# Kernel optimization log

Hardware: AMD Instinct MI355X
Metric: run time of the kernel (lower is better)

The kernel has to match this reference:

```python
import jax, jax.numpy as jnp
import numpy as np
import math

N_HEADS = 4


def setup_inputs() -> dict:
    key = jax.random.key(0)
    ks = jax.random.split(key, 5)
    Bs, M, T, C = 4, 190, 512, 64
    x = jax.random.normal(ks[0], (Bs, M, T, C), dtype=jnp.float32)
    s = 1.0 / math.sqrt(C)
    Wq = jax.random.normal(ks[1], (C, C), dtype=jnp.float32) * s
    Wk = jax.random.normal(ks[2], (C, C), dtype=jnp.float32) * s
    Wv = jax.random.normal(ks[3], (C, C), dtype=jnp.float32) * s
    Wp = jax.random.normal(ks[4], (C, C), dtype=jnp.float32) * s
    z = jnp.zeros((C,), dtype=jnp.float32)
    return {"x": x, "Wq": Wq, "bq": z, "Wk": Wk, "bk": z, "Wv": Wv, "bv": z, "Wp": Wp, "bp": z}


def reference(x, Wq, bq, Wk, bk, Wv, bv, Wp, bp):
    # AxialMultiAttention forward, tied=True, linear=False, dropout=0 (eval).
    Bs, M, T, C = x.shape
    N, D = N_HEADS, C // N_HEADS

    def heads(y):  # [Bs,M,T,C] -> [Bs,M,N,T,D]
        return y.reshape(Bs, M, T, N, D).transpose(0, 1, 3, 2, 4)

    q = heads(x @ Wq + bq)
    k = heads(x @ Wk + bk)
    v = heads(x @ Wv + bv)

    # tied: sum queries/keys over the axial (pair) dim M, keepdim -> size-1 axis
    q_t = q.sum(axis=1)  # [Bs,N,T,D]
    k_t = k.sum(axis=1)  # [Bs,N,T,D]
    scale = 1.0 / math.sqrt(D * M)
    weights = jax.nn.softmax(jnp.einsum('bnqd,bnkd->bnqk', q_t, k_t) * scale, axis=-1)  # [Bs,N,T,T]

    # broadcast tied weights across M when multiplying values
    att = jnp.einsum('bnqk,bmnkd->bmnqd', weights, v)  # [Bs,M,N,T,D]
    att = att.transpose(0, 1, 3, 2, 4).reshape(Bs, M, T, N * D)
    out = att @ Wp + bp  # [Bs,M,T,C]

    # a = weights.detach()[0].mean(0): weights has keepdim axis of size 1 in torch,
    # so [0] -> [1,N,T,T] and mean over dim 0 -> [N,T,T]
    a = jax.lax.stop_gradient(weights)[0]  # [N,T,T]
    return out, a
```

## Files before the change

kernel.cpp:

```cpp
#include <hip/hip_runtime.h>

typedef unsigned short ushort_t;
typedef __bf16 bf16x8 __attribute__((ext_vector_type(8)));
typedef float f32x4 __attribute__((ext_vector_type(4)));
typedef float f32x16 __attribute__((ext_vector_type(16)));

#define DEVI __device__ __forceinline__

constexpr int BSZ = 4;
constexpr int MDIM = 190;
constexpr int TDIM = 512;
constexpr int CDIM = 64;

DEVI ushort_t f2bf(float f) {
    union { float f; unsigned int u; } v; v.f = f;
    unsigned int u = v.u;
    u += 0x7FFFu + ((u >> 16) & 1u);
    return (ushort_t)(u >> 16);
}

__global__ __launch_bounds__(256, 4) void k_vproj(const float* __restrict__ x,
                                                  const float* __restrict__ Wv,
                                                  const float* __restrict__ bv,
                                                  ushort_t* __restrict__ vf,
                                                  float* __restrict__ xsp) {
    __shared__ __align__(16) ushort_t xbf[64 * 72];
    __shared__ __align__(16) ushort_t WvT[64 * 72];
    __shared__ __align__(16) ushort_t vst[64 * 72];

    int tid = threadIdx.x;
    int bid = blockIdx.x;
    int mg = bid & 15;
    int tt = (bid >> 4) & 7;
    int b = bid >> 7;
    int t0 = tt * 64;
    int mbase = mg * 12;
    int cnt = (mbase + 12 <= MDIM) ? 12 : (MDIM - mbase);

    int w = tid >> 6, lane = tid & 63;
    int la = lane & 15, lb = lane >> 4;
    int r = tid >> 2, seg = tid & 3;

    int chunk = tid >> 3, u = tid & 7;
    int ksr = chunk >> 3;
    int nn2 = (chunk >> 1) & 3;
    int lhi2 = chunk & 1;
    int d0 = u * 2;

#pragma unroll
    for (int rep = 0; rep < 16; ++rep) {
        int j = rep * 256 + tid;
        int ci = j >> 6, co = j & 63;
        WvT[co * 72 + ci] = f2bf(Wv[j]);
    }
    float bvv[4];
#pragma unroll
    for (int cf = 0; cf < 4; ++cf) bvv[cf] = bv[16 * cf + la];

    float xacc[16];
#pragma unroll
    for (int u2 = 0; u2 < 16; ++u2) xacc[u2] = 0.f;

    const size_t mstride = (size_t)TDIM * CDIM;
    size_t xaddr = ((size_t)(b * MDIM + mbase) * TDIM + t0 + r) * CDIM + seg * 16;

    float4 xv[4];
#pragma unroll
    for (int u2 = 0; u2 < 4; ++u2) xv[u2] = *(const float4*)(x + xaddr + u2 * 4);

    f32x4 zz = {0.f, 0.f, 0.f, 0.f};

    for (int i = 0; i < cnt; ++i) {
#pragma unroll
        for (int u2 = 0; u2 < 4; ++u2) {
            xacc[u2 * 4 + 0] += xv[u2].x;
            xacc[u2 * 4 + 1] += xv[u2].y;
            xacc[u2 * 4 + 2] += xv[u2].z;
            xacc[u2 * 4 + 3] += xv[u2].w;
            ushort4 h;
            h.x = f2bf(xv[u2].x); h.y = f2bf(xv[u2].y);
            h.z = f2bf(xv[u2].z); h.w = f2bf(xv[u2].w);
            *(ushort4*)&xbf[r * 72 + seg * 16 + u2 * 4] = h;
        }
        __syncthreads();

        int inext = (i + 1 < cnt) ? (i + 1) : i;
        size_t xaddr2 = xaddr + (size_t)(inext - i) * mstride;
        float4 xv2[4];
#pragma unroll
        for (int u2 = 0; u2 < 4; ++u2) xv2[u2] = *(const float4*)(x + xaddr2 + u2 * 4);

        f32x4 acc2[4];
#pragma unroll
        for (int cf = 0; cf < 4; ++cf) acc2[cf] = zz;
#pragma unroll
        for (int ks = 0; ks < 2; ++ks) {
            bf16x8 aa = *(const bf16x8*)&xbf[(w * 16 + la) * 72 + ks * 32 + lb * 8];
#pragma unroll
            for (int cf = 0; cf < 4; ++cf) {
                bf16x8 bb = *(const bf16x8*)&WvT[(16 * cf + la) * 72 + ks * 32 + lb * 8];
                acc2[cf] = __builtin_amdgcn_mfma_f32_16x16x32_bf16(aa, bb, acc2[cf], 0, 0, 0);
            }
        }
#pragma unroll
        for (int cf = 0; cf < 4; ++cf) {
            ushort4 h;
            h.x = f2bf(acc2[cf][0] + bvv[cf]);
            h.y = f2bf(acc2[cf][1] + bvv[cf]);
            h.z = f2bf(acc2[cf][2] + bvv[cf]);
            h.w = f2bf(acc2[cf][3] + bvv[cf]);
            *(ushort4*)&vst[(16 * cf + la) * 72 + w * 16 + lb * 4] = h;
        }
        __syncthreads();

        int m = mbase + i;
        int mblk = m >> 2, mrel = m & 3;
        int cg = mrel >> 1, half = mrel & 1;
        size_t vfbase = ((((size_t)(b * 48 + mblk) * 4 + nn2) * 32 + (tt * 4 + ksr)) * 2 + cg) * 512
                      + (size_t)(lhi2 * 32 + half * 16 + d0) * 8;
        uint4 v0 = *(const uint4*)&vst[(nn2 * 16 + d0) * 72 + ksr * 16 + lhi2 * 8];
        uint4 v1 = *(const uint4*)&vst[(nn2 * 16 + d0 + 1) * 72 + ksr * 16 + lhi2 * 8];
        *(uint4*)(vf + vfbase) = v0;
        *(uint4*)(vf + vfbase + 8) = v1;

#pragma unroll
        for (int u2 = 0; u2 < 4; ++u2) xv[u2] = xv2[u2];
        xaddr = xaddr2;
    }

    if (mg == 15) {
        uint4 z4 = {0u, 0u, 0u, 0u};
#pragma unroll
        for (int pm = 190; pm < 192; ++pm) {
            int mblk = pm >> 2, mrel = pm & 3;
            int cg = mrel >> 1, half = mrel & 1;
            size_t vfbase = ((((size_t)(b * 48 + mblk) * 4 + nn2) * 32 + (tt * 4 + ksr)) * 2 + cg) * 512
                          + (size_t)(lhi2 * 32 + half * 16 + d0) * 8;
            *(uint4*)(vf + vfbase) = z4;
            *(uint4*)(vf + vfbase + 8) = z4;
        }
    }

    size_t sbase = ((size_t)(mg * 4 + b) * TDIM + t0 + r) * CDIM + seg * 16;
#pragma unroll
    for (int u2 = 0; u2 < 4; ++u2) {
        float4 o;
        o.x = xacc[u2 * 4 + 0]; o.y = xacc[u2 * 4 + 1];
        o.z = xacc[u2 * 4 + 2]; o.w = xacc[u2 * 4 + 3];
        *(float4*)(xsp + sbase + u2 * 4) = o;
    }
}

__global__ __launch_bounds__(256) void k_xsum2(const float* __restrict__ xsp,
                                               float* __restrict__ xsum) {
    int idx = blockIdx.x * 256 + threadIdx.x;
    float s = 0.f;
#pragma unroll
    for (int p = 0; p < 16; ++p) s += xsp[(size_t)p * 131072 + idx];
    xsum[idx] = s;
}

__global__ __launch_bounds__(256) void k_weights(const float* __restrict__ xsum,
                                                 const float* __restrict__ Wq,
                                                 const float* __restrict__ bq,
                                                 const float* __restrict__ Wk,
                                                 const float* __restrict__ bk,
                                                 ushort_t* __restrict__ wf,
                                                 float* __restrict__ a_out) {
    __shared__ __align__(16) float kt[512][20];
    __shared__ __align__(16) float qt[32][20];
    __shared__ __align__(16) float xs[64][68];
    __shared__ __align__(16) float wcol[64][16];
    __shared__ float kbias[16], qbias[16];
    __shared__ __align__(16) ushort_t rowbuf[32][520];

    int tid = threadIdx.x;
    int bid = blockIdx.x;
    int tcn = bid & 15;
    int n = (bid >> 4) & 3;
    int b = bid >> 6;
    int t0 = tcn * 32;

    for (int j = tid; j < 1024; j += 256) {
        int c = j >> 4, d = j & 15;
        wcol[c][d] = Wk[c * 64 + n * 16 + d];
    }
    if (tid < 16) kbias[tid] = 190.0f * bk[n * 16 + tid];
    if (tid >= 16 && tid < 32) qbias[tid - 16] = 190.0f * bq[n * 16 + tid - 16];
    __syncthreads();

    for (int ch = 0; ch < 8; ++ch) {
        for (int j = tid; j < 4096; j += 256) {
            int t = j >> 6, c = j & 63;
            xs[t][c] = xsum[((size_t)(b * 512) + (ch * 64 + t)) * 64 + c];
        }
        __syncthreads();
#pragma unroll
        for (int o = 0; o < 4; ++o) {
            int oi = o * 256 + tid;
            int t = oi >> 4, d = oi & 15;
            float s = 0.f;
#pragma unroll
            for (int c = 0; c < 64; ++c) s += xs[t][c] * wcol[c][d];
            kt[ch * 64 + t][d] = s + kbias[d];
        }
        __syncthreads();
    }

    for (int j = tid; j < 1024; j += 256) {
        int c = j >> 4, d = j & 15;
        wcol[c][d] = Wq[c * 64 + n * 16 + d];
    }
    for (int j = tid; j < 2048; j += 256) {
        int t = j >> 6, c = j & 63;
        xs[t][c] = xsum[((size_t)(b * 512) + (t0 + t)) * 64 + c];
    }
    __syncthreads();
#pragma unroll
    for (int o = 0; o < 2; ++o) {
        int oi = o * 256 + tid;
        int t = oi >> 4, d = oi & 15;
        float s = 0.f;
#pragma unroll
        for (int c = 0; c < 64; ++c) s += xs[t][c] * wcol[c][d];
        qt[t][d] = s + qbias[d];
    }
    __syncthreads();

    const float scale = 0.01813692f;
    int w = tid >> 6, lane = tid & 63;
    for (int rr = 0; rr < 8; ++rr) {
        int r = w * 8 + rr;
        float qreg[16];
#pragma unroll
        for (int d = 0; d < 16; ++d) qreg[d] = qt[r][d];
        float lv[8];
#pragma unroll
        for (int i = 0; i < 8; ++i) {
            int k = lane + 64 * i;
            const float* kr = &kt[k][0];
            float s = 0.f;
#pragma unroll
            for (int d = 0; d < 16; ++d) s += qreg[d] * kr[d];
            lv[i] = s * scale;
        }
        float mx = lv[0];
#pragma unroll
        for (int i = 1; i < 8; ++i) mx = fmaxf(mx, lv[i]);
#pragma unroll
        for (int off = 32; off >= 1; off >>= 1) mx = fmaxf(mx, __shfl_xor(mx, off));
        float se = 0.f;
#pragma unroll
        for (int i = 0; i < 8; ++i) { lv[i] = __expf(lv[i] - mx); se += lv[i]; }
#pragma unroll
        for (int off = 32; off >= 1; off >>= 1) se += __shfl_xor(se, off);
        float inv = 1.0f / se;

        size_t abase = ((size_t)(n * 512 + (t0 + r))) * 512;
#pragma unroll
        for (int i = 0; i < 8; ++i) {
            float wv = lv[i] * inv;
            rowbuf[r][lane + 64 * i] = f2bf(wv);
            if (b == 0) a_out[abase + lane + 64 * i] = wv;
        }
    }
    __syncthreads();

    size_t wfbase = ((size_t)((b * 4 + n) * 16 + tcn)) * 32 * 512;
#pragma unroll
    for (int p = 0; p < 8; ++p) {
        int id = p * 256 + tid;
        int ks = id >> 6;
        int lf = id & 63;
        int l31 = lf & 31, lhi = lf >> 5;
        uint4 v = *(const uint4*)&rowbuf[l31][ks * 16 + lhi * 8];
        *(uint4*)(wf + wfbase + (size_t)ks * 512 + lf * 8) = v;
    }
}

__global__ __launch_bounds__(256, 2) void k_att(const ushort_t* __restrict__ wf,
                                                const ushort_t* __restrict__ vf,
                                                const float* __restrict__ Wp,
                                                const float* __restrict__ bp,
                                                float* __restrict__ out) {
    __shared__ __align__(16) ushort_t attS[4 * 64 * 68];
    __shared__ __align__(16) ushort_t WpT[64 * 68];

    int tid = threadIdx.x;
    int bid0 = blockIdx.x;
    int bid = (bid0 & 7) * 96 + (bid0 >> 3);
    int mgrp = bid % 48;
    int panel = bid / 48;
    int tt = panel & 3;
    int b = panel >> 2;

    int w = tid >> 6, lane = tid & 63;
    int l31 = lane & 31, lhi = lane >> 5;
    int n = w;

#pragma unroll
    for (int rep = 0; rep < 16; ++rep) {
        int j = rep * 256 + tid;
        int ci = j >> 6, co = j & 63;
        WpT[co * 68 + ci] = f2bf(Wp[j]);
    }

    unsigned abase[4];
#pragma unroll
    for (int q = 0; q < 4; ++q)
        abase[q] = (unsigned)((((b * 4 + n) * 16 + tt * 4 + q) * 32) * 512 + lane * 8);
    unsigned bbase[2];
#pragma unroll
    for (int j = 0; j < 2; ++j)
        bbase[j] = (unsigned)(((((b * 48 + mgrp) * 4 + n) * 32) * 2 + j) * 512 + lane * 8);

    f32x16 acc[4][2];
#pragma unroll
    for (int q = 0; q < 4; ++q)
#pragma unroll
        for (int j = 0; j < 2; ++j) acc[q][j] = (f32x16)(0.f);

    bf16x8 A0[4], B0[2], A1[4], B1[2], A2[4], B2[2];

#define LOADC(A_, B_, KS) do {                                                    \
    _Pragma("unroll")                                                             \
    for (int q = 0; q < 4; ++q)                                                   \
        A_[q] = *(const bf16x8*)(wf + abase[q] + (KS) * 512);                     \
    _Pragma("unroll")                                                             \
    for (int j = 0; j < 2; ++j)                                                   \
        B_[j] = *(const bf16x8*)(vf + bbase[j] + (KS) * 1024);                    \
} while (0)

#define COMPC(A_, B_) do {                                                        \
    _Pragma("unroll")                                                             \
    for (int q = 0; q < 4; ++q)                                                   \
        _Pragma("unroll")                                                         \
        for (int j = 0; j < 2; ++j)                                               \
            acc[q][j] = __builtin_amdgcn_mfma_f32_32x32x16_bf16(A_[q], B_[j], acc[q][j], 0, 0, 0); \
} while (0)

#define VMW(N) do { asm volatile("s_waitcnt vmcnt(" #N ")" ::: "memory"); __builtin_amdgcn_sched_barrier(0); } while (0)

    LOADC(A0, B0, 0);
    LOADC(A1, B1, 1);
    LOADC(A2, B2, 2);
#pragma unroll
    for (int g = 0; g < 9; ++g) {
        VMW(12);  COMPC(A0, B0);  LOADC(A0, B0, g * 3 + 3);
        VMW(12);  COMPC(A1, B1);  LOADC(A1, B1, g * 3 + 4);
        VMW(12);  COMPC(A2, B2);  LOADC(A2, B2, g * 3 + 5);
    }
    VMW(12);  COMPC(A0, B0);  LOADC(A0, B0, 30);
    VMW(12);  COMPC(A1, B1);  LOADC(A1, B1, 31);
    VMW(12);  COMPC(A2, B2);
    VMW(6);   COMPC(A0, B0);
    VMW(0);   COMPC(A1, B1);
#undef LOADC
#undef COMPC
#undef VMW

    float bpv[2];
#pragma unroll
    for (int cf = 0; cf < 2; ++cf) bpv[cf] = bp[cf * 32 + l31];

    int m = mgrp * 4 + w;

#pragma unroll
    for (int th = 0; th < 2; ++th) {
        __syncthreads();
#pragma unroll
        for (int qq = 0; qq < 2; ++qq)
#pragma unroll
            for (int j = 0; j < 2; ++j) {
                f32x16 a = acc[th * 2 + qq][j];
                int mloc = j * 2 + (l31 >> 4);
                int d = l31 & 15;
#pragma unroll
                for (int r = 0; r < 16; ++r) {
                    int t = qq * 32 + (r & 3) + 8 * (r >> 2) + 4 * lhi;
                    attS[(mloc * 64 + t) * 68 + n * 16 + d] = f2bf(a[r]);
                }
            }
        __syncthreads();

        size_t obase = ((size_t)(b * 190 + m) * 512 + tt * 128 + th * 64) * 64;
#pragma unroll
        for (int q2 = 0; q2 < 2; ++q2) {
            f32x16 acc2[2];
#pragma unroll
            for (int cf = 0; cf < 2; ++cf) acc2[cf] = (f32x16)(0.f);
#pragma unroll
            for (int kk = 0; kk < 4; ++kk) {
                bf16x8 aa = *(const bf16x8*)(attS + (w * 64 + q2 * 32 + l31) * 68 + kk * 16 + lhi * 8);
#pragma unroll
                for (int cf = 0; cf < 2; ++cf) {
                    bf16x8 bbf = *(const bf16x8*)(WpT + (cf * 32 + l31) * 68 + kk * 16 + lhi * 8);
                    acc2[cf] = __builtin_amdgcn_mfma_f32_32x32x16_bf16(aa, bbf, acc2[cf], 0, 0, 0);
                }
            }
            if (m < 190) {
#pragma unroll
                for (int cf = 0; cf < 2; ++cf)
#pragma unroll
                    for (int r = 0; r < 16; ++r) {
                        int t = q2 * 32 + (r & 3) + 8 * (r >> 2) + 4 * lhi;
                        int c = cf * 32 + l31;
                        out[obase + (size_t)t * 64 + c] = acc2[cf][r] + bpv[cf];
                    }
            }
        }
    }
}

extern "C" void kernel_launch(void* const* d_in, const int* in_sizes, int n_in,
                              void* d_out, int out_size, void* d_ws, size_t ws_size,
                              hipStream_t stream) {
    const float* x  = (const float*)d_in[0];
    const float* Wq = (const float*)d_in[1];
    const float* bq = (const float*)d_in[2];
    const float* Wk = (const float*)d_in[3];
    const float* bk = (const float*)d_in[4];
    const float* Wv = (const float*)d_in[5];
    const float* bv = (const float*)d_in[6];
    const float* Wp = (const float*)d_in[7];
    const float* bp = (const float*)d_in[8];

    float* out = (float*)d_out;
    float* a_out = out + (size_t)BSZ * MDIM * TDIM * CDIM;

    float* xsp = out;

    float* xsum = (float*)d_ws;
    ushort_t* wf = (ushort_t*)((char*)d_ws + 524288);
    ushort_t* vf = (ushort_t*)((char*)d_ws + 524288 + 8388608);

    k_vproj<<<512, 256, 0, stream>>>(x, Wv, bv, vf, xsp);
    k_xsum2<<<512, 256, 0, stream>>>(xsp, xsum);
    k_weights<<<256, 256, 0, stream>>>(xsum, Wq, bq, Wk, bk, wf, a_out);
    k_att<<<768, 256, 0, stream>>>(wf, vf, Wp, bp, out);
}
```

Before: 123.2 us.

## Restructure attention-value kernel into 1024-thread blocks with LDS-staged V tiles

The k_att kernel now uses 1024-thread blocks, each covering half of T for a group of four M slices. The V operand is staged into shared memory with global_load_lds, so the 16 waves share it instead of each loading from global memory. The output projection now goes through a swizzled LDS buffer written in four phases. The explicit triple-buffered register prefetch pipeline is gone, and there are more block-wide syncs, so global-load latency on the weight operand may be less well hidden.

```diff
diff --git a/kernel.cpp b/kernel.cpp
--- a/kernel.cpp
+++ b/kernel.cpp
@@ -17,6 +17,12 @@
     unsigned int u = v.u;
     u += 0x7FFFu + ((u >> 16) & 1u);
     return (ushort_t)(u >> 16);
+}
+
+DEVI void gload16(ushort_t* ldsBase, const ushort_t* g) {
+    __builtin_amdgcn_global_load_lds(
+        (const __attribute__((address_space(1))) unsigned int*)g,
+        (__attribute__((address_space(3))) unsigned int*)ldsBase, 16, 0, 0);
 }
 
 __global__ __launch_bounds__(256, 4) void k_vproj(const float* __restrict__ x,
@@ -278,138 +284,116 @@
     }
 }
 
-__global__ __launch_bounds__(256, 2) void k_att(const ushort_t* __restrict__ wf,
-                                                const ushort_t* __restrict__ vf,
-                                                const float* __restrict__ Wp,
-                                                const float* __restrict__ bp,
-                                                float* __restrict__ out) {
-    __shared__ __align__(16) ushort_t attS[4 * 64 * 68];
-    __shared__ __align__(16) ushort_t WpT[64 * 68];
+__global__ __launch_bounds__(1024, 4) void k_att(const ushort_t* __restrict__ wf,
+                                                 const ushort_t* __restrict__ vf,
+                                                 const float* __restrict__ Wp,
+                                                 const float* __restrict__ bp,
+                                                 float* __restrict__ out) {
+    __shared__ __align__(16) ushort_t arena[32768];
 
     int tid = threadIdx.x;
     int bid0 = blockIdx.x;
-    int bid = (bid0 & 7) * 96 + (bid0 >> 3);
-    int mgrp = bid % 48;
-    int panel = bid / 48;
-    int tt = panel & 3;
-    int b = panel >> 2;
-
-    int w = tid >> 6, lane = tid & 63;
+    int bid = (bid0 & 7) * 48 + (bid0 >> 3);
+    int mq = bid % 48;
+    int pane = bid / 48;
+    int th = pane & 1;
+    int b = pane >> 1;
+
+    int wid = tid >> 6, lane = tid & 63;
     int l31 = lane & 31, lhi = lane >> 5;
-    int n = w;
-
-#pragma unroll
-    for (int rep = 0; rep < 16; ++rep) {
-        int j = rep * 256 + tid;
+    int n = wid >> 2;
+    int cg = (wid >> 1) & 1;
+    int tq = wid & 1;
+
+    int ksl0 = (tid >> 7) & 7;
+    int cg0 = (tid >> 6) & 1;
+    int lane0 = tid & 63;
+    unsigned vsrc[4];
+#pragma unroll
+    for (int p = 0; p < 4; ++p)
+        vsrc[p] = (unsigned)(((((b * 48 + mq) * 4 + p) * 32 + ksl0) * 2 + cg0) * 512 + lane0 * 8);
+    ushort_t* vdst[4];
+#pragma unroll
+    for (int p = 0; p < 4; ++p) vdst[p] = arena + (p * 1024 + tid) * 8;
+
+    unsigned abase[4];
+#pragma unroll
+    for (int q = 0; q < 4; ++q)
+        abase[q] = (unsigned)((((b * 4 + n) * 16 + th * 8 + tq * 4 + q) * 32) * 512 + lane * 8);
+
+    int boff = ((n * 8) * 2 + cg) * 512 + lane * 8;
+
+    f32x16 acc[4];
+#pragma unroll
+    for (int q = 0; q < 4; ++q) acc[q] = (f32x16)(0.f);
+
+    for (int c = 0; c < 4; ++c) {
+        if (c) __syncthreads();
+#pragma unroll
+        for (int p = 0; p < 4; ++p) gload16(vdst[p], vf + vsrc[p] + c * 8192);
+        __syncthreads();
+#pragma unroll
+        for (int ksl = 0; ksl < 8; ++ksl) {
+            int ks = c * 8 + ksl;
+            bf16x8 bb = *(const bf16x8*)(arena + boff + ksl * 1024);
+#pragma unroll
+            for (int q = 0; q < 4; ++q) {
+                bf16x8 aa = *(const bf16x8*)(wf + abase[q] + ks * 512);
+                acc[q] = __builtin_amdgcn_mfma_f32_32x32x16_bf16(aa, bb, acc[q], 0, 0, 0);
+            }
+        }
+    }
+
+    __syncthreads();
+#pragma unroll
+    for (int p = 0; p < 4; ++p) {
+        int j = p * 1024 + tid;
         int ci = j >> 6, co = j & 63;
-        WpT[co * 68 + ci] = f2bf(Wp[j]);
-    }
-
-    unsigned abase[4];
-#pragma unroll
-    for (int q = 0; q < 4; ++q)
-        abase[q] = (unsigned)((((b * 4 + n) * 16 + tt * 4 + q) * 32) * 512 + lane * 8);
-    unsigned bbase[2];
-#pragma unroll
-    for (int j = 0; j < 2; ++j)
-        bbase[j] = (unsigned)(((((b * 48 + mgrp) * 4 + n) * 32) * 2 + j) * 512 + lane * 8);
-
-    f32x16 acc[4][2];
-#pragma unroll
-    for (int q = 0; q < 4; ++q)
-#pragma unroll
-        for (int j = 0; j < 2; ++j) acc[q][j] = (f32x16)(0.f);
-
-    bf16x8 A0[4], B0[2], A1[4], B1[2], A2[4], B2[2];
-
-#define LOADC(A_, B_, KS) do {                                                    \
-    _Pragma("unroll")                                                             \
-    for (int q = 0; q < 4; ++q)                                                   \
-        A_[q] = *(const bf16x8*)(wf + abase[q] + (KS) * 512);                     \
-    _Pragma("unroll")                                                             \
-    for (int j = 0; j < 2; ++j)                                                   \
-        B_[j] = *(const bf16x8*)(vf + bbase[j] + (KS) * 1024);                    \
-} while (0)
-
-#define COMPC(A_, B_) do {                                                        \
-    _Pragma("unroll")                                                             \
-    for (int q = 0; q < 4; ++q)                                                   \
-        _Pragma("unroll")                                                         \
-        for (int j = 0; j < 2; ++j)                                               \
-            acc[q][j] = __builtin_amdgcn_mfma_f32_32x32x16_bf16(A_[q], B_[j], acc[q][j], 0, 0, 0); \
-} while (0)
-
-#define VMW(N) do { asm volatile("s_waitcnt vmcnt(" #N ")" ::: "memory"); __builtin_amdgcn_sched_barrier(0); } while (0)
-
-    LOADC(A0, B0, 0);
-    LOADC(A1, B1, 1);
-    LOADC(A2, B2, 2);
-#pragma unroll
-    for (int g = 0; g < 9; ++g) {
-        VMW(12);  COMPC(A0, B0);  LOADC(A0, B0, g * 3 + 3);
-        VMW(12);  COMPC(A1, B1);  LOADC(A1, B1, g * 3 + 4);
-        VMW(12);  COMPC(A2, B2);  LOADC(A2, B2, g * 3 + 5);
-    }
-    VMW(12);  COMPC(A0, B0);  LOADC(A0, B0, 30);
-    VMW(12);  COMPC(A1, B1);  LOADC(A1, B1, 31);
-    VMW(12);  COMPC(A2, B2);
-    VMW(6);   COMPC(A0, B0);
-    VMW(0);   COMPC(A1, B1);
-#undef LOADC
-#undef COMPC
-#undef VMW
-
-    float bpv[2];
-#pragma unroll
-    for (int cf = 0; cf < 2; ++cf) bpv[cf] = bp[cf * 32 + l31];
-
-    int m = mgrp * 4 + w;
-
-#pragma unroll
-    for (int th = 0; th < 2; ++th) {
-        __syncthreads();
-#pragma unroll
-        for (int qq = 0; qq < 2; ++qq)
-#pragma unroll
-            for (int j = 0; j < 2; ++j) {
-                f32x16 a = acc[th * 2 + qq][j];
-                int mloc = j * 2 + (l31 >> 4);
-                int d = l31 & 15;
-#pragma unroll
-                for (int r = 0; r < 16; ++r) {
-                    int t = qq * 32 + (r & 3) + 8 * (r >> 2) + 4 * lhi;
-                    attS[(mloc * 64 + t) * 68 + n * 16 + d] = f2bf(a[r]);
+        arena[co * 68 + ci] = f2bf(Wp[j]);
+    }
+    ushort_t* attS = arena + 4352;
+
+    int mloc2 = wid >> 3, rt = (wid >> 1) & 3, cf = wid & 1;
+    float bpv = bp[cf * 32 + l31];
+
+#pragma unroll
+    for (int pcg = 0; pcg < 2; ++pcg)
+#pragma unroll
+        for (int pth = 0; pth < 2; ++pth) {
+            __syncthreads();
+            if (cg == pcg && tq == pth) {
+                int mloc = l31 >> 4, d = l31 & 15;
+#pragma unroll
+                for (int q = 0; q < 4; ++q) {
+                    f32x16 a = acc[q];
+#pragma unroll
+                    for (int r = 0; r < 16; ++r) {
+                        int ts = q * 32 + (r & 3) + 8 * (r >> 2) + 4 * lhi;
+                        int idx = (((mloc * 128 + ts) * 64) + n * 16 + d) ^ ((ts & 7) << 3);
+                        attS[idx] = f2bf(a[r]);
+                    }
                 }
             }
-        __syncthreads();
-
-        size_t obase = ((size_t)(b * 190 + m) * 512 + tt * 128 + th * 64) * 64;
-#pragma unroll
-        for (int q2 = 0; q2 < 2; ++q2) {
-            f32x16 acc2[2];
-#pragma unroll
-            for (int cf = 0; cf < 2; ++cf) acc2[cf] = (f32x16)(0.f);
+            __syncthreads();
+
+            f32x16 a2 = (f32x16)(0.f);
 #pragma unroll
             for (int kk = 0; kk < 4; ++kk) {
-                bf16x8 aa = *(const bf16x8*)(attS + (w * 64 + q2 * 32 + l31) * 68 + kk * 16 + lhi * 8);
-#pragma unroll
-                for (int cf = 0; cf < 2; ++cf) {
-                    bf16x8 bbf = *(const bf16x8*)(WpT + (cf * 32 + l31) * 68 + kk * 16 + lhi * 8);
-                    acc2[cf] = __builtin_amdgcn_mfma_f32_32x32x16_bf16(aa, bbf, acc2[cf], 0, 0, 0);
+                int aoff = (((mloc2 * 128 + rt * 32 + l31) * 64) + kk * 16 + lhi * 8) ^ ((l31 & 7) << 3);
+                bf16x8 aa = *(const bf16x8*)(attS + aoff);
+                bf16x8 bb = *(const bf16x8*)(arena + (cf * 32 + l31) * 68 + kk * 16 + lhi * 8);
+                a2 = __builtin_amdgcn_mfma_f32_32x32x16_bf16(aa, bb, a2, 0, 0, 0);
+            }
+            int m = mq * 4 + pcg * 2 + mloc2;
+            if (m < 190) {
+                size_t obase = ((size_t)(b * 190 + m) * 512 + th * 256 + pth * 128 + rt * 32) * 64;
+#pragma unroll
+                for (int r = 0; r < 16; ++r) {
+                    int trow = (r & 3) + 8 * (r >> 2) + 4 * lhi;
+                    out[obase + (size_t)trow * 64 + cf * 32 + l31] = a2[r] + bpv;
                 }
             }
-            if (m < 190) {
-#pragma unroll
-                for (int cf = 0; cf < 2; ++cf)
-#pragma unroll
-                    for (int r = 0; r < 16; ++r) {
-                        int t = q2 * 32 + (r & 3) + 8 * (r >> 2) + 4 * lhi;
-                        int c = cf * 32 + l31;
-                        out[obase + (size_t)t * 64 + c] = acc2[cf][r] + bpv[cf];
-                    }
-            }
-        }
-    }
+        }
 }
 
 extern "C" void kernel_launch(void* const* d_in, const int* in_sizes, int n_in,
@@ -437,5 +421,5 @@
     k_vproj<<<512, 256, 0, stream>>>(x, Wv, bv, vf, xsp);
     k_xsum2<<<512, 256, 0, stream>>>(xsp, xsum);
     k_weights<<<256, 256, 0, stream>>>(xsum, Wq, bq, Wk, bk, wf, a_out);
-    k_att<<<768, 256, 0, stream>>>(wf, vf, Wp, bp, out);
-}
+    k_att<<<384, 1024, 0, stream>>>(wf, vf, Wp, bp, out);
+}
```

Result: slower. 183.2 us (+48.8%).

## Double k_att block size, share attention tiles across two m-halves, prepack Wp fragments

Applied to the files above, without the earlier changes.

The attention kernel now runs 512-thread blocks, each covering two m-blocks. Pairs of waves share the same head's weight-row loads, so total blocks drop from 768 to 384. Wp is converted to bf16 MFMA fragment layout once in k_xsum2 and read from global memory, replacing the per-block transpose into LDS. The attS buffer uses an XOR swizzle instead of padding. The prefetch pipeline goes from triple to double buffering, which reduces register pressure under the larger block but gives less latency hiding.

```diff
diff --git a/kernel.cpp b/kernel.cpp
--- a/kernel.cpp
+++ b/kernel.cpp
@@ -152,12 +152,24 @@
 }
 
 __global__ __launch_bounds__(256) void k_xsum2(const float* __restrict__ xsp,
-                                               float* __restrict__ xsum) {
-    int idx = blockIdx.x * 256 + threadIdx.x;
+                                               const float* __restrict__ Wp,
+                                               float* __restrict__ xsum,
+                                               ushort_t* __restrict__ wpf) {
+    int tid = threadIdx.x;
+    int idx = blockIdx.x * 256 + tid;
     float s = 0.f;
 #pragma unroll
     for (int p = 0; p < 16; ++p) s += xsp[(size_t)p * 131072 + idx];
     xsum[idx] = s;
+
+    if (blockIdx.x == 0) {
+#pragma unroll
+        for (int rp = 0; rp < 16; ++rp) {
+            int u = rp * 256 + tid;
+            int cf = u >> 11, kk = (u >> 9) & 3, lf = (u >> 3) & 63, j = u & 7;
+            wpf[u] = f2bf(Wp[(kk * 16 + (lf >> 5) * 8 + j) * 64 + cf * 32 + (lf & 31)]);
+        }
+    }
 }
 
 __global__ __launch_bounds__(256) void k_weights(const float* __restrict__ xsum,
@@ -278,32 +290,26 @@
     }
 }
 
-__global__ __launch_bounds__(256, 2) void k_att(const ushort_t* __restrict__ wf,
+__global__ __launch_bounds__(512, 2) void k_att(const ushort_t* __restrict__ wf,
                                                 const ushort_t* __restrict__ vf,
-                                                const float* __restrict__ Wp,
+                                                const ushort_t* __restrict__ wpf,
                                                 const float* __restrict__ bp,
                                                 float* __restrict__ out) {
-    __shared__ __align__(16) ushort_t attS[4 * 64 * 68];
-    __shared__ __align__(16) ushort_t WpT[64 * 68];
+    __shared__ __align__(16) ushort_t attS[32768];
 
     int tid = threadIdx.x;
     int bid0 = blockIdx.x;
-    int bid = (bid0 & 7) * 96 + (bid0 >> 3);
-    int mgrp = bid % 48;
-    int panel = bid / 48;
+    int bid = (bid0 & 7) * 48 + (bid0 >> 3);
+    int mq = bid % 24;
+    int panel = bid / 24;
     int tt = panel & 3;
     int b = panel >> 2;
 
-    int w = tid >> 6, lane = tid & 63;
+    int wid = tid >> 6, lane = tid & 63;
     int l31 = lane & 31, lhi = lane >> 5;
-    int n = w;
-
-#pragma unroll
-    for (int rep = 0; rep < 16; ++rep) {
-        int j = rep * 256 + tid;
-        int ci = j >> 6, co = j & 63;
-        WpT[co * 68 + ci] = f2bf(Wp[j]);
-    }
+    int n = wid >> 1;
+    int mh = wid & 1;
+    int mblk = mq * 2 + mh;
 
     unsigned abase[4];
 #pragma unroll
@@ -312,7 +318,7 @@
     unsigned bbase[2];
 #pragma unroll
     for (int j = 0; j < 2; ++j)
-        bbase[j] = (unsigned)(((((b * 48 + mgrp) * 4 + n) * 32) * 2 + j) * 512 + lane * 8);
+        bbase[j] = (unsigned)(((((b * 48 + mblk) * 4 + n) * 32) * 2 + j) * 512 + lane * 8);
 
     f32x16 acc[4][2];
 #pragma unroll
@@ -320,7 +326,7 @@
 #pragma unroll
         for (int j = 0; j < 2; ++j) acc[q][j] = (f32x16)(0.f);
 
-    bf16x8 A0[4], B0[2], A1[4], B1[2], A2[4], B2[2];
+    bf16x8 Ae[4], Be[2], Ao[4], Bo[2];
 
 #define LOADC(A_, B_, KS) do {                                                    \
     _Pragma("unroll")                                                             \
@@ -333,28 +339,23 @@
 
 #define COMPC(A_, B_) do {                                                        \
     _Pragma("unroll")                                                             \
-    for (int q = 0; q < 4; ++q)                                                   \
+    for (int j = 0; j < 2; ++j)                                                   \
         _Pragma("unroll")                                                         \
-        for (int j = 0; j < 2; ++j)                                               \
+        for (int q = 0; q < 4; ++q)                                               \
             acc[q][j] = __builtin_amdgcn_mfma_f32_32x32x16_bf16(A_[q], B_[j], acc[q][j], 0, 0, 0); \
 } while (0)
 
 #define VMW(N) do { asm volatile("s_waitcnt vmcnt(" #N ")" ::: "memory"); __builtin_amdgcn_sched_barrier(0); } while (0)
 
-    LOADC(A0, B0, 0);
-    LOADC(A1, B1, 1);
-    LOADC(A2, B2, 2);
-#pragma unroll
-    for (int g = 0; g < 9; ++g) {
-        VMW(12);  COMPC(A0, B0);  LOADC(A0, B0, g * 3 + 3);
-        VMW(12);  COMPC(A1, B1);  LOADC(A1, B1, g * 3 + 4);
-        VMW(12);  COMPC(A2, B2);  LOADC(A2, B2, g * 3 + 5);
-    }
-    VMW(12);  COMPC(A0, B0);  LOADC(A0, B0, 30);
-    VMW(12);  COMPC(A1, B1);  LOADC(A1, B1, 31);
-    VMW(12);  COMPC(A2, B2);
-    VMW(6);   COMPC(A0, B0);
-    VMW(0);   COMPC(A1, B1);
+    LOADC(Ae, Be, 0);
+    LOADC(Ao, Bo, 1);
+#pragma unroll
+    for (int kc = 0; kc < 30; kc += 2) {
+        VMW(6);  COMPC(Ae, Be);  LOADC(Ae, Be, kc + 2);
+        VMW(6);  COMPC(Ao, Bo);  LOADC(Ao, Bo, kc + 3);
+    }
+    VMW(6);  COMPC(Ae, Be);
+    VMW(0);  COMPC(Ao, Bo);
 #undef LOADC
 #undef COMPC
 #undef VMW
@@ -363,51 +364,64 @@
 #pragma unroll
     for (int cf = 0; cf < 2; ++cf) bpv[cf] = bp[cf * 32 + l31];
 
-    int m = mgrp * 4 + w;
-
-#pragma unroll
-    for (int th = 0; th < 2; ++th) {
-        __syncthreads();
-#pragma unroll
-        for (int qq = 0; qq < 2; ++qq)
-#pragma unroll
-            for (int j = 0; j < 2; ++j) {
-                f32x16 a = acc[th * 2 + qq][j];
-                int mloc = j * 2 + (l31 >> 4);
-                int d = l31 & 15;
-#pragma unroll
-                for (int r = 0; r < 16; ++r) {
-                    int t = qq * 32 + (r & 3) + 8 * (r >> 2) + 4 * lhi;
-                    attS[(mloc * 64 + t) * 68 + n * 16 + d] = f2bf(a[r]);
+    int mloc2 = wid >> 1;
+    int th2 = wid & 1;
+
+#pragma unroll
+    for (int h = 0; h < 2; ++h) {
+        __syncthreads();
+        if (mh == h) {
+            int mloc = ((l31 >> 4));
+            int d = l31 & 15;
+#pragma unroll
+            for (int cg = 0; cg < 2; ++cg)
+#pragma unroll
+                for (int q = 0; q < 4; ++q) {
+                    f32x16 a = acc[q][cg];
+                    int ml = cg * 2 + mloc;
+#pragma unroll
+                    for (int r = 0; r < 16; ++r) {
+                        int tl = q * 32 + (r & 3) + 8 * (r >> 2) + 4 * lhi;
+                        int idx = (((ml * 128 + tl) * 64) + n * 16 + d) ^ ((tl & 7) << 3);
+                        attS[idx] = f2bf(a[r]);
+                    }
                 }
+        }
+        __syncthreads();
+
+        f32x16 acc2[2][2];
+#pragma unroll
+        for (int q2 = 0; q2 < 2; ++q2)
+#pragma unroll
+            for (int cf = 0; cf < 2; ++cf) acc2[q2][cf] = (f32x16)(0.f);
+#pragma unroll
+        for (int kk = 0; kk < 4; ++kk) {
+            bf16x8 bbf[2];
+#pragma unroll
+            for (int cf = 0; cf < 2; ++cf)
+                bbf[cf] = *(const bf16x8*)(wpf + (cf * 4 + kk) * 512 + lane * 8);
+#pragma unroll
+            for (int q2 = 0; q2 < 2; ++q2) {
+                int tl = th2 * 64 + q2 * 32 + l31;
+                int aidx = (((mloc2 * 128 + tl) * 64) + kk * 16 + lhi * 8) ^ ((tl & 7) << 3);
+                bf16x8 aa = *(const bf16x8*)(attS + aidx);
+#pragma unroll
+                for (int cf = 0; cf < 2; ++cf)
+                    acc2[q2][cf] = __builtin_amdgcn_mfma_f32_32x32x16_bf16(aa, bbf[cf], acc2[q2][cf], 0, 0, 0);
             }
-        __syncthreads();
-
-        size_t obase = ((size_t)(b * 190 + m) * 512 + tt * 128 + th * 64) * 64;
-#pragma unroll
-        for (int q2 = 0; q2 < 2; ++q2) {
-            f32x16 acc2[2];
-#pragma unroll
-            for (int cf = 0; cf < 2; ++cf) acc2[cf] = (f32x16)(0.f);
-#pragma unroll
-            for (int kk = 0; kk < 4; ++kk) {
-                bf16x8 aa = *(const bf16x8*)(attS + (w * 64 + q2 * 32 + l31) * 68 + kk * 16 + lhi * 8);
-#pragma unroll
-                for (int cf = 0; cf < 2; ++cf) {
-                    bf16x8 bbf = *(const bf16x8*)(WpT + (cf * 32 + l31) * 68 + kk * 16 + lhi * 8);
-                    acc2[cf] = __builtin_amdgcn_mfma_f32_32x32x16_bf16(aa, bbf, acc2[cf], 0, 0, 0);
-                }
-            }
-            if (m < 190) {
+        }
+        int m = mq * 8 + h * 4 + mloc2;
+        if (m < 190) {
+            size_t obase = ((size_t)(b * 190 + m) * 512 + tt * 128 + th2 * 64) * 64;
+#pragma unroll
+            for (int q2 = 0; q2 < 2; ++q2)
 #pragma unroll
                 for (int cf = 0; cf < 2; ++cf)
 #pragma unroll
                     for (int r = 0; r < 16; ++r) {
-                        int t = q2 * 32 + (r & 3) + 8 * (r >> 2) + 4 * lhi;
-                        int c = cf * 32 + l31;
-                        out[obase + (size_t)t * 64 + c] = acc2[cf][r] + bpv[cf];
+                        int ts = q2 * 32 + (r & 3) + 8 * (r >> 2) + 4 * lhi;
+                        out[obase + (size_t)ts * 64 + cf * 32 + l31] = acc2[q2][cf][r] + bpv[cf];
                     }
-            }
         }
     }
 }
@@ -433,9 +447,10 @@
     float* xsum = (float*)d_ws;
     ushort_t* wf = (ushort_t*)((char*)d_ws + 524288);
     ushort_t* vf = (ushort_t*)((char*)d_ws + 524288 + 8388608);
+    ushort_t* wpf = (ushort_t*)((char*)d_ws + 524288 + 8388608 + 50331648);
 
     k_vproj<<<512, 256, 0, stream>>>(x, Wv, bv, vf, xsp);
-    k_xsum2<<<512, 256, 0, stream>>>(xsp, xsum);
+    k_xsum2<<<512, 256, 0, stream>>>(xsp, Wp, xsum, wpf);
     k_weights<<<256, 256, 0, stream>>>(xsum, Wq, bq, Wk, bk, wf, a_out);
-    k_att<<<768, 256, 0, stream>>>(wf, vf, Wp, bp, out);
-}
+    k_att<<<384, 512, 0, stream>>>(wf, vf, wpf, bp, out);
+}
```

Result: slower. 140.6 us (+14.1%).
